# Performance work log

Measured on AMD Instinct MI355X. Metric: run time of the kernel, lower is better.

The kernel has to match this reference:

```python
import jax, jax.numpy as jnp
import numpy as np
import math

B, S, D, H = 4, 2048, 1024, 16
HD = D // H  # 64

def setup_inputs() -> dict:
    key = jax.random.key(0)
    ks = jax.random.split(key, 4)
    x = jax.random.normal(ks[0], (B, S, D), dtype=jnp.float32)
    # causal mask, True = attend (precomputed as in the original usage)
    mask = jnp.tril(jnp.ones((S, S), dtype=bool))[None, None, :, :]
    c_attn_w = jax.random.normal(ks[1], (D, 3 * D), dtype=jnp.float32) * 0.02
    c_attn_b = jnp.zeros((3 * D,), dtype=jnp.float32)
    c_proj_w = jax.random.normal(ks[2], (D, D), dtype=jnp.float32) * 0.02
    c_proj_b = jnp.zeros((D,), dtype=jnp.float32)
    return {"x": x, "mask": mask, "c_attn_w": c_attn_w, "c_attn_b": c_attn_b,
            "c_proj_w": c_proj_w, "c_proj_b": c_proj_b}

def reference(x, mask, c_attn_w, c_attn_b, c_proj_w, c_proj_b):
    b, s, d = x.shape
    # c_attn: Conv1D acts as Linear with transposed weight convention
    qkv = x @ c_attn_w + c_attn_b                      # [B,S,3D]
    q, k, v = jnp.split(qkv, 3, axis=-1)
    q = q.reshape(b, s, H, HD).transpose(0, 2, 1, 3)   # [B,H,S,hd]
    k = k.reshape(b, s, H, HD).transpose(0, 2, 1, 3)   # [B,H,S,hd]
    v = v.reshape(b, s, H, HD).transpose(0, 2, 1, 3)   # [B,H,S,hd]
    # scores, scale by sqrt(head_dim) (done unconditionally in _attn)
    w = jnp.einsum('bhqd,bhkd->bhqk', q, k) / math.sqrt(HD)
    # masked_fill_(1 - mask, -10000.0)
    w = jnp.where(mask, w, jnp.float32(-10000.0))
    w = jax.nn.softmax(w, axis=-1)                     # attn_dropout p=0
    a = jnp.einsum('bhqk,bhkd->bhqd', w, v)            # [B,H,S,hd]
    a = a.transpose(0, 2, 1, 3).reshape(b, s, d)       # merge heads
    out = a @ c_proj_w + c_proj_b                      # resid_dropout p=0
    return out
```

## Files before the change

### kernel.cpp

```cpp
#include <hip/hip_runtime.h>

#define SEQ  2048
#define DIM  1024
#define NH   16
#define HD   64
#define NB   4

typedef __bf16 bf16_t;
typedef bf16_t bf16x8 __attribute__((ext_vector_type(8)));
typedef bf16_t bf16x4 __attribute__((ext_vector_type(4)));
typedef float  floatx4 __attribute__((ext_vector_type(4)));

#define MFMA16(a, b, c) __builtin_amdgcn_mfma_f32_16x16x32_bf16((a), (b), (c), 0, 0, 0)

__device__ __forceinline__ void gl_lds16(const bf16_t* g, bf16_t* l) {
    __builtin_amdgcn_global_load_lds(
        (const __attribute__((address_space(1))) void*)g,
        (__attribute__((address_space(3))) void*)l,
        16, 0, 0);
}

__global__ __launch_bounds__(256) void prep(
    const float* __restrict__ x, bf16_t* __restrict__ xb,
    const float* __restrict__ wqkv, bf16_t* __restrict__ wqkvT,
    const float* __restrict__ wproj, bf16_t* __restrict__ wprojT) {
    const int bid = blockIdx.x, tid = threadIdx.x;
    if (bid < 8192) {
        const int i = (bid * 256 + tid) * 4;
        const float4 v = *(const float4*)(x + i);
        xb[i + 0] = (bf16_t)v.x;
        xb[i + 1] = (bf16_t)v.y;
        xb[i + 2] = (bf16_t)v.z;
        xb[i + 3] = (bf16_t)v.w;
        return;
    }
    __shared__ bf16_t t[32][33];
    const float* in;
    bf16_t* out;
    int R, C, bx, by;
    if (bid < 8192 + 3072) {
        const int idx = bid - 8192;
        in = wqkv; out = wqkvT; R = 1024; C = 3072;
        bx = idx % 96; by = idx / 96;
    } else {
        const int idx = bid - 11264;
        in = wproj; out = wprojT; R = 1024; C = 1024;
        bx = idx & 31; by = idx >> 5;
    }
    const int c0 = bx * 32, r0 = by * 32;
    const int tx = tid & 31, ty = tid >> 5;
#pragma unroll
    for (int i = 0; i < 32; i += 8)
        t[ty + i][tx] = (bf16_t)in[(r0 + ty + i) * C + c0 + tx];
    __syncthreads();
#pragma unroll
    for (int i = 0; i < 32; i += 8)
        out[(c0 + ty + i) * R + r0 + tx] = t[tx][ty + i];
}

template <int MODE>
__global__ __launch_bounds__(256, 2) void gemm128(
    const bf16_t* __restrict__ A, const bf16_t* __restrict__ Bt,
    const float* __restrict__ bias, int K,
    bf16_t* __restrict__ Qo, bf16_t* __restrict__ Ko, bf16_t* __restrict__ Vo,
    float* __restrict__ Co) {
    __shared__ __align__(16) bf16_t smem[MODE == 0 ? 128 * 136 : 128 * 128];
    bf16_t* Al = smem;
    bf16_t* Bl = smem + 128 * 64;

    const int tid = threadIdx.x;
    const int m0 = blockIdx.y * 128, n0 = blockIdx.x * 128;
    const int w = tid >> 6, lane = tid & 63;
    const int l15 = lane & 15, quad = lane >> 4;
    const int wm = (w & 1) * 64, wn = (w >> 1) * 64;

    floatx4 acc[4][4] = {};

    const int g_st = ((tid & 7) - (tid >> 3)) & 7;
    const bf16_t* aptr = A + (m0 + (tid >> 3)) * K + g_st * 8;
    const bf16_t* bptr = Bt + (n0 + (tid >> 3)) * K + g_st * 8;
    bf16_t* al = Al + tid * 8;
    bf16_t* bl = Bl + tid * 8;

    for (int k0 = 0; k0 < K; k0 += 64) {
#pragma unroll
        for (int c = 0; c < 4; c++) {
            gl_lds16(aptr + (c * 32) * K, al + c * 2048);
            gl_lds16(bptr + (c * 32) * K, bl + c * 2048);
        }
        aptr += 64;
        bptr += 64;
        __syncthreads();

#pragma unroll
        for (int h = 0; h < 2; h++) {
            const int sAB = (((h << 2) + quad + (l15 & 7)) & 7) * 8;
            bf16x8 af[4], bfr[4];
#pragma unroll
            for (int i = 0; i < 4; i++)
                af[i] = *(const bf16x8*)&Al[(wm + i * 16 + l15) * 64 + sAB];
#pragma unroll
            for (int j = 0; j < 4; j++)
                bfr[j] = *(const bf16x8*)&Bl[(wn + j * 16 + l15) * 64 + sAB];
#pragma unroll
            for (int i = 0; i < 4; i++)
#pragma unroll
                for (int j = 0; j < 4; j++)
                    acc[i][j] = MODE == 0 ? MFMA16(bfr[j], af[i], acc[i][j])
                                          : MFMA16(af[i], bfr[j], acc[i][j]);
        }
        __syncthreads();
    }

    if (MODE == 0) {
        bf16_t* Cl = smem;
        const int which = n0 >> 10;
        const float qs = (which == 0) ? 0.18033688f : 1.0f;
#pragma unroll
        for (int j = 0; j < 4; j++) {
            const int nc = wn + j * 16 + quad * 4;
#pragma unroll
            for (int i = 0; i < 4; i++) {
                const int mrow = wm + i * 16 + l15;
                bf16x4 pk;
#pragma unroll
                for (int r = 0; r < 4; r++)
                    pk[r] = (bf16_t)((acc[i][j][r] + bias[n0 + nc + r]) * qs);
                *(bf16x4*)&Cl[mrow * 136 + nc] = pk;
            }
        }
        __syncthreads();

        if (which < 2) {
            const int row = tid >> 1, ch = (tid & 1) << 6;
            const int m = m0 + row, b = m >> 11, s = m & 2047;
            const int h = ((n0 & 1023) >> 6) + (ch >> 6);
            bf16_t* dst = (which == 0 ? Qo : Ko) + ((size_t)(b * NH + h) * SEQ + s) * HD;
            const bf16_t* src = Cl + row * 136 + ch;
#pragma unroll
            for (int g = 0; g < 8; g++)
                *(bf16x8*)(dst + g * 8) = *(const bf16x8*)(src + g * 8);
        } else {
            const int dl = tid & 127, sh = (tid >> 7) << 6;
            const int h = ((n0 & 1023) >> 6) + (dl >> 6), d = dl & 63;
            const int b = m0 >> 11, sbase = (m0 & 2047) + sh;
            bf16_t* dst = Vo + ((size_t)(b * NH + h) * HD + d) * SEQ + sbase;
#pragma unroll
            for (int g = 0; g < 8; g++) {
                bf16x8 tv;
#pragma unroll
                for (int e = 0; e < 8; e++)
                    tv[e] = Cl[(sh + g * 8 + e) * 136 + dl];
                *(bf16x8*)(dst + g * 8) = tv;
            }
        }
    } else {
#pragma unroll
        for (int j = 0; j < 4; j++) {
            const int n = n0 + wn + j * 16 + l15;
            const float bv = bias[n];
#pragma unroll
            for (int i = 0; i < 4; i++)
#pragma unroll
                for (int r = 0; r < 4; r++) {
                    const int m = m0 + wm + i * 16 + quad * 4 + r;
                    Co[m * 1024 + n] = acc[i][j][r] + bv;
                }
        }
    }
}

__global__ __launch_bounds__(256, 3) void attn1q(
    const bf16_t* __restrict__ Q, const bf16_t* __restrict__ Kg,
    const bf16_t* __restrict__ Vt, bf16_t* __restrict__ Aout) {
    __shared__ __align__(16) bf16_t Ks[2 * 64 * 64];
    __shared__ __align__(16) bf16_t Vs[2 * 64 * 64];
    __shared__ __align__(16) bf16_t Ps[128 * 64];

    const int bh = blockIdx.x;
    const int qt = 15 - blockIdx.y;
    const int nk = 2 * qt + 2;

    const int tid = threadIdx.x, w = tid >> 6, lane = tid & 63;
    const int l15 = lane & 15, quad = lane >> 4;
    const int b = bh >> 4, hd = bh & 15;
    const int xk = l15 & 7;

    bf16x8 aq[2][2];
#pragma unroll
    for (int i = 0; i < 2; i++) {
        const bf16_t* qr = Q + (size_t)(bh * SEQ + qt * 128 + w * 32 + i * 16 + l15) * HD;
#pragma unroll
        for (int h = 0; h < 2; h++)
            aq[i][h] = *(const bf16x8*)(qr + h * 32 + quad * 8);
    }

    floatx4 o[2][4] = {};
    float li[2] = {};

    const int srow = tid >> 3;
    const int sg = (tid & 7) ^ (srow & 7);
    const bf16_t* kgl = Kg + (size_t)bh * SEQ * HD + (size_t)srow * HD + sg * 8;
    const bf16_t* vgl = Vt + (size_t)bh * HD * SEQ + (size_t)srow * SEQ + sg * 8;

    auto stage = [&](int buf, int kt) {
        const bf16_t* kp = kgl + kt * (64 * HD);
        const bf16_t* vp = vgl + kt * 64;
        bf16_t* kd = Ks + buf * 4096 + tid * 8;
        bf16_t* vd = Vs + buf * 4096 + tid * 8;
        gl_lds16(kp, kd);
        gl_lds16(kp + 32 * HD, kd + 2048);
        gl_lds16(vp, vd);
        gl_lds16(vp + 32 * SEQ, vd + 2048);
    };

    auto proc = [&](int kt, int buf) {
        const bf16_t* Ksub = Ks + buf * 4096;
        const bf16_t* Vsub = Vs + buf * 4096;
        bf16x8 bk[4][2];
#pragma unroll
        for (int j = 0; j < 4; j++) {
            const int n = j * 16 + l15;
#pragma unroll
            for (int h = 0; h < 2; h++)
                bk[j][h] = *(const bf16x8*)&Ksub[n * 64 + (((h * 4 + quad) ^ xk) * 8)];
        }
        floatx4 z[2][4] = {};
        __builtin_amdgcn_s_setprio(1);
#pragma unroll
        for (int i = 0; i < 2; i++)
#pragma unroll
            for (int j = 0; j < 4; j++) {
                z[i][j] = MFMA16(bk[j][0], aq[i][0], z[i][j]);
                z[i][j] = MFMA16(bk[j][1], aq[i][1], z[i][j]);
            }
        __builtin_amdgcn_s_setprio(0);
#pragma unroll
        for (int i = 0; i < 2; i++) {
            const int qbase = qt * 128 + w * 32 + i * 16;
            const int qrow_l = qbase + l15;
            const bool full = (kt * 64 + 63) <= qbase;
            const int prow = w * 32 + i * 16 + l15;
            bf16_t* pbase = Ps + prow * 64;
            const int rx = prow & 7;
#pragma unroll
            for (int j = 0; j < 4; j++) {
                const int kg0 = kt * 64 + j * 16 + quad * 4;
                bf16x4 pk;
                float es[4];
#pragma unroll
                for (int r = 0; r < 4; r++) {
                    float e = __builtin_amdgcn_exp2f(z[i][j][r]);
                    if (!full && kg0 + r > qrow_l) e = 0.f;
                    es[r] = e;
                    pk[r] = (bf16_t)e;
                }
                li[i] += (es[0] + es[1]) + (es[2] + es[3]);
                const int g = 2 * j + (quad >> 1);
                *(bf16x4*)(pbase + (((g ^ rx) << 3) | ((quad & 1) << 2))) = pk;
            }
        }
        __builtin_amdgcn_s_waitcnt(0xC07F);
        bf16x8 ap[2][2];
#pragma unroll
        for (int i = 0; i < 2; i++) {
            const int row = w * 32 + i * 16 + l15;
#pragma unroll
            for (int kk = 0; kk < 2; kk++)
                ap[i][kk] = *(const bf16x8*)&Ps[row * 64 +
                                               (((kk * 4 + quad) ^ (row & 7)) << 3)];
        }
        bf16x8 bv[4][2];
#pragma unroll
        for (int j = 0; j < 4; j++) {
            const int n = j * 16 + l15;
#pragma unroll
            for (int kk = 0; kk < 2; kk++)
                bv[j][kk] = *(const bf16x8*)&Vsub[n * 64 + (((kk * 4 + quad) ^ xk) * 8)];
        }
        __builtin_amdgcn_s_setprio(1);
#pragma unroll
        for (int i = 0; i < 2; i++)
#pragma unroll
            for (int j = 0; j < 4; j++) {
                o[i][j] = MFMA16(ap[i][0], bv[j][0], o[i][j]);
                o[i][j] = MFMA16(ap[i][1], bv[j][1], o[i][j]);
            }
        __builtin_amdgcn_s_setprio(0);
    };

    stage(0, 0);
    __syncthreads();
    for (int kt = 0; kt < nk; ++kt) {
        const int cur = kt & 1;
        if (kt + 1 < nk) stage(cur ^ 1, kt + 1);
        proc(kt, cur);
        __syncthreads();
    }

#pragma unroll
    for (int i = 0; i < 2; i++) {
        float s = li[i];
        s += __shfl_xor(s, 16, 64);
        s += __shfl_xor(s, 32, 64);
#pragma unroll
        for (int r = 0; r < 4; r++) {
            const float sv = __shfl(s, quad * 4 + r, 64);
            const float inv = 1.0f / sv;
            const int srow_o = qt * 128 + w * 32 + i * 16 + quad * 4 + r;
            bf16_t* orow = Aout + (size_t)(b * SEQ + srow_o) * DIM + hd * HD;
#pragma unroll
            for (int j = 0; j < 4; j++)
                orow[j * 16 + l15] = (bf16_t)(o[i][j][r] * inv);
        }
    }
}

extern "C" void kernel_launch(void* const* d_in, const int* in_sizes, int n_in,
                              void* d_out, int out_size, void* d_ws, size_t ws_size,
                              hipStream_t stream) {
    const float* x        = (const float*)d_in[0];
    const float* c_attn_w = (const float*)d_in[2];
    const float* c_attn_b = (const float*)d_in[3];
    const float* c_proj_w = (const float*)d_in[4];
    const float* c_proj_b = (const float*)d_in[5];
    float* out = (float*)d_out;

    char* ws = (char*)d_ws;
    bf16_t* xb     = (bf16_t*)ws; ws += (size_t)NB * SEQ * DIM * 2;
    bf16_t* wqkvT  = (bf16_t*)ws; ws += (size_t)3072 * 1024 * 2;
    bf16_t* wprojT = (bf16_t*)ws; ws += (size_t)1024 * 1024 * 2;
    bf16_t* Qb  = (bf16_t*)ws; ws += (size_t)NB * NH * SEQ * HD * 2;
    bf16_t* Kb  = (bf16_t*)ws; ws += (size_t)NB * NH * SEQ * HD * 2;
    bf16_t* Vtb = (bf16_t*)ws; ws += (size_t)NB * NH * SEQ * HD * 2;
    bf16_t* Ab  = (bf16_t*)ws; ws += (size_t)NB * SEQ * DIM * 2;

    prep<<<12288, 256, 0, stream>>>(x, xb, c_attn_w, wqkvT, c_proj_w, wprojT);

    gemm128<0><<<dim3(24, 64), 256, 0, stream>>>(xb, wqkvT, c_attn_b, 1024,
                                                 Qb, Kb, Vtb, nullptr);

    attn1q<<<dim3(NB * NH, 16), 256, 0, stream>>>(Qb, Kb, Vtb, Ab);

    gemm128<1><<<dim3(8, 64), 256, 0, stream>>>(Ab, wprojT, c_proj_b, 1024,
                                                nullptr, nullptr, nullptr, out);
}
```

Baseline: 260.0 us.

## Replace QKV GEMM with 256x256 tiled, double-buffered, phase-pipelined kernel

Adds a new QKV projection kernel that computes 256x256 output tiles with 512 threads and double-buffered LDS filled by direct global-to-LDS loads. The main loop is split into phases that interleave the next tile's loads with MFMA work, using explicit vmcnt waits, barriers and setprio. Blocks are remapped for L2 locality. The aim is better data reuse and hiding of global-load latency in the largest GEMM. In exchange it uses 128KB of LDS and a hand-tuned barrier schedule, and the head-split epilogue now runs in two halves.

```diff
diff --git a/kernel.cpp b/kernel.cpp
--- a/kernel.cpp
+++ b/kernel.cpp
@@ -19,6 +19,10 @@
         (__attribute__((address_space(3))) void*)l,
         16, 0, 0);
 }
+
+#define VM4 asm volatile("s_waitcnt vmcnt(4)" ::: "memory")
+#define VM0 asm volatile("s_waitcnt vmcnt(0)" ::: "memory")
+#define NOPS ((void)0)
 
 __global__ __launch_bounds__(256) void prep(
     const float* __restrict__ x, bf16_t* __restrict__ xb,
@@ -58,13 +62,171 @@
         out[(c0 + ty + i) * R + r0 + tx] = t[tx][ty + i];
 }
 
+__global__ __launch_bounds__(512, 2) void gemm256_qkv(
+    const bf16_t* __restrict__ A, const bf16_t* __restrict__ Bt,
+    const float* __restrict__ bias, int K,
+    bf16_t* __restrict__ Qo, bf16_t* __restrict__ Ko, bf16_t* __restrict__ Vo) {
+    __shared__ __align__(16) bf16_t smem[65536];
+    bf16_t* As = smem;
+    bf16_t* Bs = smem + 32768;
+
+    const int bid = blockIdx.x;
+    const int swz = (bid & 7) * 48 + (bid >> 3);
+    const int m0 = (swz / 12) * 256, n0 = (swz % 12) * 256;
+
+    const int tid = threadIdx.x;
+    const int w = tid >> 6, lane = tid & 63;
+    const int l15 = lane & 15, quad = lane >> 4;
+    const int wr = w >> 2, wc = w & 3;
+    const int xk = l15 & 7;
+
+    floatx4 acc[8][4] = {};
+
+    const int strow = tid >> 3;
+    const int stg = ((tid & 7) - strow) & 7;
+    const bf16_t* aA = A + (size_t)(m0 + strow) * K + stg * 8;
+    const bf16_t* aB = Bt + (size_t)(n0 + strow) * K + stg * 8;
+
+    auto stA = [&](int buf, int kt, int h) {
+        const bf16_t* p = aA + ((size_t)h * 128) * K + kt * 64;
+        bf16_t* d = As + buf * 16384 + h * 8192 + tid * 8;
+        gl_lds16(p, d);
+        gl_lds16(p + (size_t)64 * K, d + 4096);
+    };
+    auto stB = [&](int buf, int kt, int h) {
+        const bf16_t* p = aB + ((size_t)h * 128) * K + kt * 64;
+        bf16_t* d = Bs + buf * 16384 + h * 8192 + tid * 8;
+        gl_lds16(p, d);
+        gl_lds16(p + (size_t)64 * K, d + 4096);
+    };
+
+    const bf16_t* Awave0 = As + wr * 8192;
+    const bf16_t* Bwave0 = Bs + (wc >> 1) * 8192 + (wc & 1) * 4096;
+
+    bf16x8 bfr[4][2];
+
+#define PHASE(BUF, Q, STAGE, VMW)                                              \
+    do {                                                                       \
+        const bf16_t* Ab_ = Awave0 + (BUF) * 16384;                            \
+        const bf16_t* Bb_ = Bwave0 + (BUF) * 16384;                            \
+        if ((Q) == 0) {                                                        \
+            _Pragma("unroll") for (int j_ = 0; j_ < 4; j_++)                   \
+                _Pragma("unroll") for (int kk_ = 0; kk_ < 2; kk_++)            \
+                    bfr[j_][kk_] = *(const bf16x8*)&Bb_[(j_ * 16 + l15) * 64 + \
+                        (((kk_ * 4 + quad) + xk) & 7) * 8];                    \
+        }                                                                      \
+        bf16x8 af_[2][2];                                                      \
+        _Pragma("unroll") for (int di_ = 0; di_ < 2; di_++)                    \
+            _Pragma("unroll") for (int kk_ = 0; kk_ < 2; kk_++)                \
+                af_[di_][kk_] = *(const bf16x8*)&Ab_[(((Q) * 2 + di_) * 16 + l15) * 64 + \
+                    (((kk_ * 4 + quad) + xk) & 7) * 8];                        \
+        STAGE;                                                                 \
+        VMW;                                                                   \
+        asm volatile("" ::: "memory");                                         \
+        __builtin_amdgcn_s_barrier();                                          \
+        asm volatile("s_waitcnt lgkmcnt(0)" ::: "memory");                     \
+        __builtin_amdgcn_s_setprio(1);                                         \
+        _Pragma("unroll") for (int di_ = 0; di_ < 2; di_++)                    \
+            _Pragma("unroll") for (int j_ = 0; j_ < 4; j_++) {                 \
+                acc[(Q) * 2 + di_][j_] =                                       \
+                    MFMA16(bfr[j_][0], af_[di_][0], acc[(Q) * 2 + di_][j_]);   \
+                acc[(Q) * 2 + di_][j_] =                                       \
+                    MFMA16(bfr[j_][1], af_[di_][1], acc[(Q) * 2 + di_][j_]);   \
+            }                                                                  \
+        __builtin_amdgcn_s_setprio(0);                                         \
+        asm volatile("" ::: "memory");                                         \
+        __builtin_amdgcn_s_barrier();                                          \
+        asm volatile("" ::: "memory");                                         \
+    } while (0)
+
+    const int NT = K >> 6;
+    const int NI = NT >> 1;
+
+    stA(0, 0, 0); stA(0, 0, 1); stB(0, 0, 0); stB(0, 0, 1);
+    stB(1, 1, 0); stB(1, 1, 1);
+    VM4;
+    asm volatile("" ::: "memory");
+    __builtin_amdgcn_s_barrier();
+    asm volatile("" ::: "memory");
+
+    for (int it = 0; it < NI - 1; ++it) {
+        const int T1 = 2 * it + 1, T2 = 2 * it + 2, T3 = 2 * it + 3;
+        PHASE(0, 0, stA(1, T1, 0), NOPS);
+        PHASE(0, 1, stA(1, T1, 1), NOPS);
+        PHASE(0, 2, stB(0, T2, 0), NOPS);
+        PHASE(0, 3, stB(0, T2, 1), VM4);
+        PHASE(1, 0, stA(0, T2, 0), NOPS);
+        PHASE(1, 1, stA(0, T2, 1), NOPS);
+        PHASE(1, 2, stB(1, T3, 0), NOPS);
+        PHASE(1, 3, stB(1, T3, 1), VM4);
+    }
+    {
+        PHASE(0, 0, stA(1, NT - 1, 0), NOPS);
+        PHASE(0, 1, stA(1, NT - 1, 1), NOPS);
+        PHASE(0, 2, NOPS, NOPS);
+        PHASE(0, 3, NOPS, VM0);
+        PHASE(1, 0, NOPS, NOPS);
+        PHASE(1, 1, NOPS, NOPS);
+        PHASE(1, 2, NOPS, NOPS);
+        PHASE(1, 3, NOPS, NOPS);
+    }
+#undef PHASE
+
+    bf16_t* Et = smem;
+    const int which = n0 >> 10;
+    const float qs = (which == 0) ? 0.18033688f : 1.0f;
+#pragma unroll
+    for (int c = 0; c < 2; ++c) {
+        if (c) __syncthreads();
+        if (wr == c) {
+#pragma unroll
+            for (int j = 0; j < 4; j++) {
+                const int nc = wc * 64 + j * 16 + quad * 4;
+#pragma unroll
+                for (int i = 0; i < 8; i++) {
+                    const int mrow = i * 16 + l15;
+                    bf16x4 pk;
+#pragma unroll
+                    for (int r = 0; r < 4; r++)
+                        pk[r] = (bf16_t)((acc[i][j][r] + bias[n0 + nc + r]) * qs);
+                    *(bf16x4*)&Et[mrow * 264 + nc] = pk;
+                }
+            }
+        }
+        __syncthreads();
+        if (which < 2) {
+            const int row = tid >> 2, seg = tid & 3;
+            const int m = m0 + c * 128 + row, b = m >> 11, s = m & 2047;
+            const int h = ((n0 & 1023) >> 6) + seg;
+            bf16_t* dst = (which == 0 ? Qo : Ko) + ((size_t)(b * NH + h) * SEQ + s) * HD;
+            const bf16_t* src = Et + row * 264 + seg * 64;
+#pragma unroll
+            for (int g = 0; g < 8; g++)
+                *(bf16x8*)(dst + g * 8) = *(const bf16x8*)(src + g * 8);
+        } else {
+            const int line = tid >> 1, sh = (tid & 1) << 6;
+            const int seg = line >> 6, d = line & 63;
+            const int h = ((n0 & 1023) >> 6) + seg;
+            const int b = m0 >> 11;
+            const int sbase = (m0 & 2047) + c * 128 + sh;
+            bf16_t* dst = Vo + ((size_t)(b * NH + h) * HD + d) * SEQ + sbase;
+#pragma unroll
+            for (int g = 0; g < 8; g++) {
+                bf16x8 tv;
+#pragma unroll
+                for (int e = 0; e < 8; e++)
+                    tv[e] = Et[(sh + g * 8 + e) * 264 + seg * 64 + d];
+                *(bf16x8*)(dst + g * 8) = tv;
+            }
+        }
+    }
+}
+
 template <int MODE>
 __global__ __launch_bounds__(256, 2) void gemm128(
     const bf16_t* __restrict__ A, const bf16_t* __restrict__ Bt,
-    const float* __restrict__ bias, int K,
-    bf16_t* __restrict__ Qo, bf16_t* __restrict__ Ko, bf16_t* __restrict__ Vo,
-    float* __restrict__ Co) {
-    __shared__ __align__(16) bf16_t smem[MODE == 0 ? 128 * 136 : 128 * 128];
+    const float* __restrict__ bias, int K, float* __restrict__ Co) {
+    __shared__ __align__(16) bf16_t smem[128 * 128];
     bf16_t* Al = smem;
     bf16_t* Bl = smem + 128 * 64;
 
@@ -106,67 +268,22 @@
             for (int i = 0; i < 4; i++)
 #pragma unroll
                 for (int j = 0; j < 4; j++)
-                    acc[i][j] = MODE == 0 ? MFMA16(bfr[j], af[i], acc[i][j])
-                                          : MFMA16(af[i], bfr[j], acc[i][j]);
+                    acc[i][j] = MFMA16(af[i], bfr[j], acc[i][j]);
         }
         __syncthreads();
     }
 
-    if (MODE == 0) {
-        bf16_t* Cl = smem;
-        const int which = n0 >> 10;
-        const float qs = (which == 0) ? 0.18033688f : 1.0f;
-#pragma unroll
-        for (int j = 0; j < 4; j++) {
-            const int nc = wn + j * 16 + quad * 4;
-#pragma unroll
-            for (int i = 0; i < 4; i++) {
-                const int mrow = wm + i * 16 + l15;
-                bf16x4 pk;
-#pragma unroll
-                for (int r = 0; r < 4; r++)
-                    pk[r] = (bf16_t)((acc[i][j][r] + bias[n0 + nc + r]) * qs);
-                *(bf16x4*)&Cl[mrow * 136 + nc] = pk;
-            }
-        }
-        __syncthreads();
-
-        if (which < 2) {
-            const int row = tid >> 1, ch = (tid & 1) << 6;
-            const int m = m0 + row, b = m >> 11, s = m & 2047;
-            const int h = ((n0 & 1023) >> 6) + (ch >> 6);
-            bf16_t* dst = (which == 0 ? Qo : Ko) + ((size_t)(b * NH + h) * SEQ + s) * HD;
-            const bf16_t* src = Cl + row * 136 + ch;
-#pragma unroll
-            for (int g = 0; g < 8; g++)
-                *(bf16x8*)(dst + g * 8) = *(const bf16x8*)(src + g * 8);
-        } else {
-            const int dl = tid & 127, sh = (tid >> 7) << 6;
-            const int h = ((n0 & 1023) >> 6) + (dl >> 6), d = dl & 63;
-            const int b = m0 >> 11, sbase = (m0 & 2047) + sh;
-            bf16_t* dst = Vo + ((size_t)(b * NH + h) * HD + d) * SEQ + sbase;
-#pragma unroll
-            for (int g = 0; g < 8; g++) {
-                bf16x8 tv;
-#pragma unroll
-                for (int e = 0; e < 8; e++)
-                    tv[e] = Cl[(sh + g * 8 + e) * 136 + dl];
-                *(bf16x8*)(dst + g * 8) = tv;
-            }
-        }
-    } else {
-#pragma unroll
-        for (int j = 0; j < 4; j++) {
-            const int n = n0 + wn + j * 16 + l15;
-            const float bv = bias[n];
-#pragma unroll
-            for (int i = 0; i < 4; i++)
-#pragma unroll
-                for (int r = 0; r < 4; r++) {
-                    const int m = m0 + wm + i * 16 + quad * 4 + r;
-                    Co[m * 1024 + n] = acc[i][j][r] + bv;
-                }
-        }
+#pragma unroll
+    for (int j = 0; j < 4; j++) {
+        const int n = n0 + wn + j * 16 + l15;
+        const float bv = bias[n];
+#pragma unroll
+        for (int i = 0; i < 4; i++)
+#pragma unroll
+            for (int r = 0; r < 4; r++) {
+                const int m = m0 + wm + i * 16 + quad * 4 + r;
+                Co[m * 1024 + n] = acc[i][j][r] + bv;
+            }
     }
 }
 
@@ -337,11 +454,10 @@
 
     prep<<<12288, 256, 0, stream>>>(x, xb, c_attn_w, wqkvT, c_proj_w, wprojT);
 
-    gemm128<0><<<dim3(24, 64), 256, 0, stream>>>(xb, wqkvT, c_attn_b, 1024,
-                                                 Qb, Kb, Vtb, nullptr);
+    gemm256_qkv<<<384, 512, 0, stream>>>(xb, wqkvT, c_attn_b, 1024,
+                                         Qb, Kb, Vtb);
 
     attn1q<<<dim3(NB * NH, 16), 256, 0, stream>>>(Qb, Kb, Vtb, Ab);
 
-    gemm128<1><<<dim3(8, 64), 256, 0, stream>>>(Ab, wprojT, c_proj_b, 1024,
-                                                nullptr, nullptr, nullptr, out);
-}
+    gemm128<1><<<dim3(8, 64), 256, 0, stream>>>(Ab, wprojT, c_proj_b, 1024, out);
+}
```

After: 259.1 us. Within noise of the previous version (-0.4%).
